# Performance work log

Hardware: AMD Instinct MI355X
Metric: run time of the kernel (lower is better)

## Reference

```python
import jax, jax.numpy as jnp
import numpy as np

N_NODES = 100000
N_EDGES = 1600000
D = 64
L = 3


def setup_inputs() -> dict:
    key = jax.random.key(0)
    ks = jax.random.split(key, 6)
    x = jax.random.normal(ks[0], (N_NODES, D), dtype=jnp.float32)
    edges = jax.random.randint(ks[1], (2, N_EDGES), 0, N_NODES, dtype=jnp.int64)
    scale = 1.0 / np.sqrt(D)
    W_phi = jax.random.normal(ks[2], (L, D, D), dtype=jnp.float32) * scale
    W_theta = jax.random.normal(ks[3], (L, D, D), dtype=jnp.float32) * scale
    W_out = jax.random.normal(ks[4], (1, D), dtype=jnp.float32) * scale
    b_out = jax.random.normal(ks[5], (1,), dtype=jnp.float32) * scale
    return {"x": x, "edges": edges, "W_phi": W_phi, "W_theta": W_theta,
            "W_out": W_out, "b_out": b_out}


def _devconv(x, Wp, Wt, src, dst):
    # DevConv: out_i = W_theta @ max_{j in N(i)} W_phi (x_j - x_i)
    diff = x[src] - x[dst]                 # [E, D] irregular gather
    msg = diff @ Wp.T                      # [E, D]
    agg = jax.ops.segment_max(msg, dst, num_segments=N_NODES)  # [N, D]
    agg = jnp.where(jnp.isneginf(agg), 0.0, agg)  # isolated nodes -> 0
    return agg @ Wt.T


def reference(x, edges, W_phi, W_theta, W_out, b_out):
    src, dst = edges[0], edges[1]
    for l in range(L):
        x = _devconv(x, W_phi[l], W_theta[l], src, dst)
    scores = (x @ W_out.T + b_out)[:, 0]   # Linear(D,1) then squeeze(-1)
    return jax.nn.sigmoid(scores)
```

## Files before the change

kernel.cpp:

```cpp
#include <hip/hip_runtime.h>
#include <math.h>


#define WBITS 9
#define WNODES 512
#define MAXNB 256
#define CHUNK 8192
#define STG_CAP 12288

#define PKNINF 0xFC00FC00u

typedef __fp16 h2v __attribute__((ext_vector_type(2)));
typedef _Float16 f16x8 __attribute__((ext_vector_type(8)));
typedef float f32x4 __attribute__((ext_vector_type(4)));

__device__ __forceinline__ unsigned pkmax(unsigned a, unsigned b) {
    unsigned r;
    asm("v_pk_max_f16 %0, %1, %2" : "=v"(r) : "v"(a), "v"(b));
    return r;
}
__device__ __forceinline__ unsigned pkrtz(float a, float b) {
    h2v r = __builtin_amdgcn_cvt_pkrtz(a, b);
    return *reinterpret_cast<unsigned*>(&r);
}
__device__ __forceinline__ float h2lo(unsigned u) {
    h2v h = *reinterpret_cast<h2v*>(&u);
    return (float)h.x;
}
__device__ __forceinline__ float h2hi(unsigned u) {
    h2v h = *reinterpret_cast<h2v*>(&u);
    return (float)h.y;
}

#define G8(K0) do { \
    int j0 = __builtin_amdgcn_ds_swizzle(myc, (((K0)+0)<<5)|0x10); \
    int j1 = __builtin_amdgcn_ds_swizzle(myc, (((K0)+1)<<5)|0x10); \
    int j2 = __builtin_amdgcn_ds_swizzle(myc, (((K0)+2)<<5)|0x10); \
    int j3 = __builtin_amdgcn_ds_swizzle(myc, (((K0)+3)<<5)|0x10); \
    int j4 = __builtin_amdgcn_ds_swizzle(myc, (((K0)+4)<<5)|0x10); \
    int j5 = __builtin_amdgcn_ds_swizzle(myc, (((K0)+5)<<5)|0x10); \
    int j6 = __builtin_amdgcn_ds_swizzle(myc, (((K0)+6)<<5)|0x10); \
    int j7 = __builtin_amdgcn_ds_swizzle(myc, (((K0)+7)<<5)|0x10); \
    uint2 w0 = y16[(size_t)j0 * 16 + t]; \
    uint2 w1 = y16[(size_t)j1 * 16 + t]; \
    uint2 w2 = y16[(size_t)j2 * 16 + t]; \
    uint2 w3 = y16[(size_t)j3 * 16 + t]; \
    uint2 w4 = y16[(size_t)j4 * 16 + t]; \
    uint2 w5 = y16[(size_t)j5 * 16 + t]; \
    uint2 w6 = y16[(size_t)j6 * 16 + t]; \
    uint2 w7 = y16[(size_t)j7 * 16 + t]; \
    c0 = pkmax(c0, pkmax(pkmax(pkmax(w0.x, w1.x), pkmax(w2.x, w3.x)), \
                         pkmax(pkmax(w4.x, w5.x), pkmax(w6.x, w7.x)))); \
    c1 = pkmax(c1, pkmax(pkmax(pkmax(w0.y, w1.y), pkmax(w2.y, w3.y)), \
                         pkmax(pkmax(w4.y, w5.y), pkmax(w6.y, w7.y)))); \
} while (0)

__global__ __launch_bounds__(256) void prep_k(
    const float* __restrict__ Wp, const float* __restrict__ Wt,
    const float* __restrict__ Wout,
    __fp16* __restrict__ Wh, float* __restrict__ vout)
{
    __shared__ float A[4096];
    __shared__ float B[4096];
    int tid = threadIdx.x;
    int b = blockIdx.x;
    if (b < 2) {
        const float* Ap = Wp + (size_t)(b + 1) * 4096;
        const float* Bp = Wt + (size_t)b * 4096;
        for (int i = tid; i < 4096; i += 256) { A[i] = Ap[i]; B[i] = Bp[i]; }
        __syncthreads();
        __fp16* C = Wh + (size_t)(b + 1) * 4096;
        for (int i = tid; i < 4096; i += 256) {
            int d = i >> 6, k = i & 63;
            float s = 0.f;
            #pragma unroll
            for (int m = 0; m < 64; ++m) s += A[d * 64 + m] * B[m * 64 + k];
            C[i] = (__fp16)s;
        }
    } else {
        for (int i = tid; i < 4096; i += 256) {
            A[i] = Wt[2 * 4096 + i];
            Wh[i] = (__fp16)Wp[i];
        }
        if (tid < 64) B[tid] = Wout[tid];
        __syncthreads();
        if (tid < 64) {
            float s = 0.f;
            #pragma unroll
            for (int m = 0; m < 64; ++m) s += B[m] * A[m * 64 + tid];
            vout[tid] = s;
        }
    }
}

__global__ __launch_bounds__(256) void clear_int_k(int* __restrict__ p, int n)
{
    int i = blockIdx.x * 256 + threadIdx.x;
    if (i < n) p[i] = 0;
}

__global__ __launch_bounds__(256) void bucket_hist_k(
    const int* __restrict__ eidx, int* __restrict__ bcnt, int E, int NB)
{
    __shared__ int h[MAXNB];
    int tid = threadIdx.x;
    for (int i = tid; i < NB; i += 256) h[i] = 0;
    __syncthreads();
    int start = blockIdx.x * CHUNK;
    int end = min(E, start + CHUNK);
    for (int e = start + tid; e < end; e += 256)
        atomicAdd(&h[eidx[E + e] >> WBITS], 1);
    __syncthreads();
    for (int i = tid; i < NB; i += 256)
        if (h[i]) atomicAdd(&bcnt[i], h[i]);
}

__global__ __launch_bounds__(256) void bucket_scan_k(
    const int* __restrict__ bcnt, int* __restrict__ bbase,
    int* __restrict__ gcur, int* __restrict__ row_ptr, int NB, int N, int E)
{
    __shared__ int sA[MAXNB], sB[MAXNB];
    int tid = threadIdx.x;
    int v0 = (tid < NB) ? bcnt[tid] : 0;
    sA[tid] = v0;
    __syncthreads();
    int* sp = sA; int* dp = sB;
    for (int off = 1; off < MAXNB; off <<= 1) {
        dp[tid] = sp[tid] + ((tid >= off) ? sp[tid - off] : 0);
        __syncthreads();
        int* t = sp; sp = dp; dp = t;
    }
    if (tid < NB) {
        int ex = sp[tid] - v0;
        bbase[tid] = ex;
        gcur[tid]  = ex;
    }
    if (tid == 0) {
        bbase[NB]  = E;
        row_ptr[N] = E;
    }
}

__global__ __launch_bounds__(256) void partA_k(
    const int* __restrict__ eidx, int* __restrict__ gcur,
    int* __restrict__ B1, int E, int NB)
{
    __shared__ int hist[MAXNB];
    __shared__ int lofs[MAXNB];
    __shared__ int lcur[MAXNB];
    __shared__ int gofs[MAXNB];
    __shared__ int sA[MAXNB], sB[MAXNB];
    __shared__ int stg_val[CHUNK];
    __shared__ int stg_pos[CHUNK];
    int tid = threadIdx.x;
    int start = blockIdx.x * CHUNK;
    int cnt = min(E - start, CHUNK);
    if (cnt <= 0) return;

    for (int i = tid; i < NB; i += 256) hist[i] = 0;
    __syncthreads();

    int es[CHUNK / 256], ed[CHUNK / 256];
    #pragma unroll
    for (int i = 0; i < CHUNK / 256; ++i) {
        int li = i * 256 + tid;
        if (li < cnt) {
            es[i] = eidx[start + li];
            ed[i] = eidx[E + start + li];
            atomicAdd(&hist[ed[i] >> WBITS], 1);
        }
    }
    __syncthreads();
    sA[tid] = (tid < NB) ? hist[tid] : 0;
    __syncthreads();
    int* sp = sA; int* dp = sB;
    for (int off = 1; off < MAXNB; off <<= 1) {
        dp[tid] = sp[tid] + ((tid >= off) ? sp[tid - off] : 0);
        __syncthreads();
        int* t = sp; sp = dp; dp = t;
    }
    if (tid < NB) {
        int c  = hist[tid];
        int ex = sp[tid] - c;
        lofs[tid] = ex;
        lcur[tid] = ex;
        gofs[tid] = c ? atomicAdd(&gcur[tid], c) : 0;
    }
    __syncthreads();
    #pragma unroll
    for (int i = 0; i < CHUNK / 256; ++i) {
        int li = i * 256 + tid;
        if (li < cnt) {
            int b = ed[i] >> WBITS;
            int p = atomicAdd(&lcur[b], 1);
            stg_val[p] = es[i] | ((ed[i] & (WNODES - 1)) << 17);
            stg_pos[p] = gofs[b] + (p - lofs[b]);
        }
    }
    __syncthreads();
    for (int i = tid; i < cnt; i += 256)
        B1[stg_pos[i]] = stg_val[i];
}

__global__ __launch_bounds__(256) void partB_k(
    const int* __restrict__ B1, const int* __restrict__ bbase,
    int* __restrict__ row_ptr, int* __restrict__ col, int N, int NB)
{
    __shared__ int cnt[WNODES];
    __shared__ int lcur[WNODES];
    __shared__ int sA[WNODES], sB[WNODES];
    __shared__ int stg[STG_CAP];
    int b   = blockIdx.x;
    int tid = threadIdx.x;
    int gb0 = bbase[b], gb1 = bbase[b + 1];
    int m   = gb1 - gb0;
    int nb0 = b << WBITS;

    for (int i = tid; i < WNODES; i += 256) cnt[i] = 0;
    __syncthreads();
    for (int i = tid; i < m; i += 256)
        atomicAdd(&cnt[B1[gb0 + i] >> 17], 1);
    __syncthreads();
    for (int i = tid; i < WNODES; i += 256) sA[i] = cnt[i];
    __syncthreads();
    int* sp = sA; int* dp = sB;
    for (int off = 1; off < WNODES; off <<= 1) {
        for (int i = tid; i < WNODES; i += 256)
            dp[i] = sp[i] + ((i >= off) ? sp[i - off] : 0);
        __syncthreads();
        int* t = sp; sp = dp; dp = t;
    }
    for (int i = tid; i < WNODES; i += 256) {
        int ex = sp[i] - cnt[i];
        lcur[i] = ex;
        int node = nb0 + i;
        if (node < N) row_ptr[node] = gb0 + ex;
    }
    __syncthreads();
    if (m <= STG_CAP) {
        for (int i = tid; i < m; i += 256) {
            int v = B1[gb0 + i];
            int p = atomicAdd(&lcur[v >> 17], 1);
            stg[p] = v & 0x1FFFF;
        }
        __syncthreads();
        for (int i = tid; i < m; i += 256)
            col[gb0 + i] = stg[i];
    } else {
        for (int i = tid; i < m; i += 256) {
            int v = B1[gb0 + i];
            int p = atomicAdd(&lcur[v >> 17], 1);
            col[gb0 + p] = v & 0x1FFFF;
        }
    }
}


__global__ __launch_bounds__(256) void gemm_mfma_k(
    const float* __restrict__ in, const __fp16* __restrict__ W,
    float* __restrict__ y32, unsigned short* __restrict__ y16, int n)
{
    int lane = threadIdx.x & 63;
    int wid  = threadIdx.x >> 6;
    int rt   = blockIdx.x * 4 + wid;
    int r0   = rt * 16;
    if (r0 >= n) return;

    int l15 = lane & 15;
    int ko  = (lane >> 4) * 8;

    f16x8 af[4][2];
    #pragma unroll
    for (int dt = 0; dt < 4; ++dt)
        #pragma unroll
        for (int kf = 0; kf < 2; ++kf)
            af[dt][kf] = *(const f16x8*)(W + (size_t)(dt * 16 + l15) * 64 + ko + kf * 32);

    f16x8 bf[2];
    #pragma unroll
    for (int kf = 0; kf < 2; ++kf) {
        const float4* p = (const float4*)(in + (size_t)(r0 + l15) * 64 + ko + kf * 32);
        float4 a = p[0], b = p[1];
        union { uint4 u; f16x8 h; } cv;
        cv.u.x = pkrtz(a.x, a.y); cv.u.y = pkrtz(a.z, a.w);
        cv.u.z = pkrtz(b.x, b.y); cv.u.w = pkrtz(b.z, b.w);
        bf[kf] = cv.h;
    }

    int r = r0 + l15;
    int d4 = (lane >> 4) * 4;
    #pragma unroll
    for (int dt = 0; dt < 4; ++dt) {
        f32x4 acc = {0.f, 0.f, 0.f, 0.f};
        acc = __builtin_amdgcn_mfma_f32_16x16x32_f16(af[dt][0], bf[0], acc, 0, 0, 0);
        acc = __builtin_amdgcn_mfma_f32_16x16x32_f16(af[dt][1], bf[1], acc, 0, 0, 0);
        int d = dt * 16 + d4;
        if (r < n) {
            float4 o; o.x = acc[0]; o.y = acc[1]; o.z = acc[2]; o.w = acc[3];
            *(float4*)(y32 + (size_t)r * 64 + d) = o;
            uint2 p; p.x = pkrtz(acc[0], acc[1]); p.y = pkrtz(acc[2], acc[3]);
            *(uint2*)(y16 + (size_t)r * 64 + d) = p;
        }
    }
}

template<bool HEAD>
__global__ __launch_bounds__(256) void gather_fused_k(
    const int* __restrict__ rp, const int* __restrict__ col,
    const uint2* __restrict__ y16, const float* y32,
    const __fp16* __restrict__ W,
    float* y32o, unsigned short* __restrict__ y16o,
    const float* __restrict__ vv, const float* __restrict__ bptr,
    float* __restrict__ out, int n)
{
    __shared__ __fp16 sAgg[4][16][80];
    int lane = threadIdx.x & 63;
    int wid  = threadIdx.x >> 6;
    int q = lane >> 4, t = lane & 15;
    int base = blockIdx.x * 64 + wid * 16;

    for (int p = 0; p < 4; ++p) {
        int node  = base + p * 4 + q;
        bool alive = node < n;
        int beg = 0, cnt = 0;
        if (alive) { beg = rp[node]; cnt = rp[node + 1] - beg; }
        unsigned c0 = PKNINF, c1 = PKNINF;
        if (cnt > 0) {
            int pcnt = (cnt + 7) & ~7;
            int e = 0;
            while (e < pcnt) {
                int myc = col[beg + min(e + t, cnt - 1)];
                G8(0);
                if (e + 8 < pcnt) { G8(8); }
                e += 16;
            }
        }
        if (alive) {
            bool has = cnt > 0;
            float4 yi = ((const float4*)y32)[(size_t)node * 16 + t];
            float g0 = has ? (h2lo(c0) - yi.x) : 0.f;
            float g1 = has ? (h2hi(c0) - yi.y) : 0.f;
            float g2 = has ? (h2lo(c1) - yi.z) : 0.f;
            float g3 = has ? (h2hi(c1) - yi.w) : 0.f;
            if (!HEAD) {
                uint2 pk; pk.x = pkrtz(g0, g1); pk.y = pkrtz(g2, g3);
                *(uint2*)&sAgg[wid][p * 4 + q][4 * t] = pk;
            } else {
                float4 vp = ((const float4*)vv)[t];
                float s = g0 * vp.x + g1 * vp.y + g2 * vp.z + g3 * vp.w;
                s += __shfl_xor(s, 8);
                s += __shfl_xor(s, 4);
                s += __shfl_xor(s, 2);
                s += __shfl_xor(s, 1);
                if (t == 0)
                    out[node] = 1.f / (1.f + __expf(-(s + bptr[0])));
            }
        } else if (!HEAD) {
            uint2 z; z.x = 0u; z.y = 0u;
            *(uint2*)&sAgg[wid][p * 4 + q][4 * t] = z;
        }
    }

    if (!HEAD) {
        __syncthreads();
        f16x8 af[4][2];
        #pragma unroll
        for (int dt = 0; dt < 4; ++dt)
            #pragma unroll
            for (int kf = 0; kf < 2; ++kf)
                af[dt][kf] = *(const f16x8*)(W + (size_t)(dt * 16 + t) * 64 + q * 8 + kf * 32);
        f16x8 bf[2];
        #pragma unroll
        for (int kf = 0; kf < 2; ++kf)
            bf[kf] = *(const f16x8*)&sAgg[wid][t][q * 8 + kf * 32];

        int r = base + t;
        int d4 = q * 4;
        #pragma unroll
        for (int dt = 0; dt < 4; ++dt) {
            f32x4 acc = {0.f, 0.f, 0.f, 0.f};
            acc = __builtin_amdgcn_mfma_f32_16x16x32_f16(af[dt][0], bf[0], acc, 0, 0, 0);
            acc = __builtin_amdgcn_mfma_f32_16x16x32_f16(af[dt][1], bf[1], acc, 0, 0, 0);
            if (r < n) {
                int d = dt * 16 + d4;
                float4 o; o.x = acc[0]; o.y = acc[1]; o.z = acc[2]; o.w = acc[3];
                *(float4*)(y32o + (size_t)r * 64 + d) = o;
                uint2 pk; pk.x = pkrtz(acc[0], acc[1]); pk.y = pkrtz(acc[2], acc[3]);
                *(uint2*)(y16o + (size_t)r * 64 + d) = pk;
            }
        }
    }
}

extern "C" void kernel_launch(void* const* d_in, const int* in_sizes, int n_in,
                              void* d_out, int out_size, void* d_ws, size_t ws_size,
                              hipStream_t stream)
{
    const float* x     = (const float*)d_in[0];
    const int*   edges = (const int*)d_in[1];
    const float* Wp    = (const float*)d_in[2];
    const float* Wt    = (const float*)d_in[3];
    const float* Wout  = (const float*)d_in[4];
    const float* bout  = (const float*)d_in[5];
    const int N = in_sizes[0] / 64;
    const int E = in_sizes[1] / 2;
    const int NB = (N + WNODES - 1) >> WBITS;
    float* out = (float*)d_out;

    char* ws = (char*)d_ws;
    float* y32 = (float*)ws; ws += (size_t)N * 64 * 4;
    int*   B1  = (int*)y32;
    unsigned short* y16A = (unsigned short*)ws; ws += (size_t)N * 64 * 2;
    unsigned short* y16B = (unsigned short*)ws; ws += (size_t)N * 64 * 2;
    int* col     = (int*)ws; ws += (size_t)(E + 8) * 4;
    int* row_ptr = (int*)ws; ws += (size_t)(N + 4) * 4;
    int* bcnt    = (int*)ws; ws += MAXNB * 4;
    int* bbase   = (int*)ws; ws += (MAXNB + 4) * 4;
    int* gcur    = (int*)ws; ws += MAXNB * 4;
    __fp16* Wh = (__fp16*)ws; ws += 3 * 4096 * 2;
    float*  vv = (float*)ws;  ws += 64 * 4;

    const int chunkBlocks = (E + CHUNK - 1) / CHUNK;
    const int gemmBlocks  = ((N + 15) / 16 + 3) / 4;
    const int fusedBlocks = (N + 63) / 64;

    prep_k<<<3, 256, 0, stream>>>(Wp, Wt, Wout, Wh, vv);

    clear_int_k<<<1, 256, 0, stream>>>(bcnt, NB);
    bucket_hist_k<<<chunkBlocks, 256, 0, stream>>>(edges, bcnt, E, NB);
    bucket_scan_k<<<1, 256, 0, stream>>>(bcnt, bbase, gcur, row_ptr, NB, N, E);
    partA_k<<<chunkBlocks, 256, 0, stream>>>(edges, gcur, B1, E, NB);
    partB_k<<<NB, 256, 0, stream>>>(B1, bbase, row_ptr, col, N, NB);

    gemm_mfma_k<<<gemmBlocks, 256, 0, stream>>>(x, Wh, y32, y16A, N);
    gather_fused_k<false><<<fusedBlocks, 256, 0, stream>>>(
        row_ptr, col, (const uint2*)y16A, y32, Wh + 4096, y32, y16B,
        nullptr, nullptr, nullptr, N);
    gather_fused_k<false><<<fusedBlocks, 256, 0, stream>>>(
        row_ptr, col, (const uint2*)y16B, y32, Wh + 8192, y32, y16A,
        nullptr, nullptr, nullptr, N);
    gather_fused_k<true><<<fusedBlocks, 256, 0, stream>>>(
        row_ptr, col, (const uint2*)y16A, y32, nullptr, nullptr, nullptr,
        vv, bout, out, N);
}
```

Baseline: 205.2 us.

## Drop fp32 activation buffer, fuse histogram with first GEMM, fold clear into prep

Removes the fp32 copy of each layer's transformed features. The self term x_i is now read from the fp16 buffer that is already written, which cuts a full-width write and read per layer. The edge-bucket histogram and the first-layer MFMA GEMM now run as one launch, split by block index, and clearing the bucket counts moves into the weight-prep kernel. Together these remove two launches, and the partition scratch B1 now aliases the second fp16 buffer. The trade-off is slightly lower precision in the x_i subtraction, since it now uses fp16 instead of fp32.

```diff
diff --git a/kernel.cpp b/kernel.cpp
--- a/kernel.cpp
+++ b/kernel.cpp
@@ -58,13 +58,15 @@
 __global__ __launch_bounds__(256) void prep_k(
     const float* __restrict__ Wp, const float* __restrict__ Wt,
     const float* __restrict__ Wout,
-    __fp16* __restrict__ Wh, float* __restrict__ vout)
+    __fp16* __restrict__ Wh, float* __restrict__ vout,
+    int* __restrict__ bcnt)
 {
     __shared__ float A[4096];
     __shared__ float B[4096];
     int tid = threadIdx.x;
     int b = blockIdx.x;
     if (b < 2) {
+        if (b == 0 && tid < MAXNB) bcnt[tid] = 0;
         const float* Ap = Wp + (size_t)(b + 1) * 4096;
         const float* Bp = Wt + (size_t)b * 4096;
         for (int i = tid; i < 4096; i += 256) { A[i] = Ap[i]; B[i] = Bp[i]; }
@@ -93,26 +95,64 @@
     }
 }
 
-__global__ __launch_bounds__(256) void clear_int_k(int* __restrict__ p, int n)
-{
-    int i = blockIdx.x * 256 + threadIdx.x;
-    if (i < n) p[i] = 0;
-}
-
-__global__ __launch_bounds__(256) void bucket_hist_k(
-    const int* __restrict__ eidx, int* __restrict__ bcnt, int E, int NB)
+__global__ __launch_bounds__(256) void hist_gemm_k(
+    const int* __restrict__ eidx, int* __restrict__ bcnt, int E, int NB,
+    int chunkBlocks,
+    const float* __restrict__ xin, const __fp16* __restrict__ W,
+    unsigned short* __restrict__ y16o, int n)
 {
     __shared__ int h[MAXNB];
     int tid = threadIdx.x;
-    for (int i = tid; i < NB; i += 256) h[i] = 0;
-    __syncthreads();
-    int start = blockIdx.x * CHUNK;
-    int end = min(E, start + CHUNK);
-    for (int e = start + tid; e < end; e += 256)
-        atomicAdd(&h[eidx[E + e] >> WBITS], 1);
-    __syncthreads();
-    for (int i = tid; i < NB; i += 256)
-        if (h[i]) atomicAdd(&bcnt[i], h[i]);
+    if (blockIdx.x < chunkBlocks) {
+        for (int i = tid; i < NB; i += 256) h[i] = 0;
+        __syncthreads();
+        int start = blockIdx.x * CHUNK;
+        int end = min(E, start + CHUNK);
+        for (int e = start + tid; e < end; e += 256)
+            atomicAdd(&h[eidx[E + e] >> WBITS], 1);
+        __syncthreads();
+        for (int i = tid; i < NB; i += 256)
+            if (h[i]) atomicAdd(&bcnt[i], h[i]);
+    } else {
+        int lane = tid & 63;
+        int wid  = tid >> 6;
+        int r0   = ((blockIdx.x - chunkBlocks) * 4 + wid) * 16;
+        if (r0 >= n) return;
+        int l15 = lane & 15;
+        int ko  = (lane >> 4) * 8;
+
+        f16x8 af[4][2];
+        #pragma unroll
+        for (int dt = 0; dt < 4; ++dt)
+            #pragma unroll
+            for (int kf = 0; kf < 2; ++kf)
+                af[dt][kf] = *(const f16x8*)(W + (size_t)(dt * 16 + l15) * 64 + ko + kf * 32);
+
+        f16x8 bf[2];
+        int rr = min(r0 + l15, n - 1);
+        #pragma unroll
+        for (int kf = 0; kf < 2; ++kf) {
+            const float4* p = (const float4*)(xin + (size_t)rr * 64 + ko + kf * 32);
+            float4 a = p[0], b = p[1];
+            union { uint4 u; f16x8 hh; } cv;
+            cv.u.x = pkrtz(a.x, a.y); cv.u.y = pkrtz(a.z, a.w);
+            cv.u.z = pkrtz(b.x, b.y); cv.u.w = pkrtz(b.z, b.w);
+            bf[kf] = cv.hh;
+        }
+
+        int r = r0 + l15;
+        int d4 = (lane >> 4) * 4;
+        #pragma unroll
+        for (int dt = 0; dt < 4; ++dt) {
+            f32x4 acc = {0.f, 0.f, 0.f, 0.f};
+            acc = __builtin_amdgcn_mfma_f32_16x16x32_f16(af[dt][0], bf[0], acc, 0, 0, 0);
+            acc = __builtin_amdgcn_mfma_f32_16x16x32_f16(af[dt][1], bf[1], acc, 0, 0, 0);
+            if (r < n) {
+                uint2 p; p.x = pkrtz(acc[0], acc[1]); p.y = pkrtz(acc[2], acc[3]);
+                *(uint2*)(y16o + (size_t)r * 64 + dt * 16 + d4) = p;
+            }
+        }
+    }
 }
 
 __global__ __launch_bounds__(256) void bucket_scan_k(
@@ -255,61 +295,12 @@
     }
 }
 
-
-__global__ __launch_bounds__(256) void gemm_mfma_k(
-    const float* __restrict__ in, const __fp16* __restrict__ W,
-    float* __restrict__ y32, unsigned short* __restrict__ y16, int n)
-{
-    int lane = threadIdx.x & 63;
-    int wid  = threadIdx.x >> 6;
-    int rt   = blockIdx.x * 4 + wid;
-    int r0   = rt * 16;
-    if (r0 >= n) return;
-
-    int l15 = lane & 15;
-    int ko  = (lane >> 4) * 8;
-
-    f16x8 af[4][2];
-    #pragma unroll
-    for (int dt = 0; dt < 4; ++dt)
-        #pragma unroll
-        for (int kf = 0; kf < 2; ++kf)
-            af[dt][kf] = *(const f16x8*)(W + (size_t)(dt * 16 + l15) * 64 + ko + kf * 32);
-
-    f16x8 bf[2];
-    #pragma unroll
-    for (int kf = 0; kf < 2; ++kf) {
-        const float4* p = (const float4*)(in + (size_t)(r0 + l15) * 64 + ko + kf * 32);
-        float4 a = p[0], b = p[1];
-        union { uint4 u; f16x8 h; } cv;
-        cv.u.x = pkrtz(a.x, a.y); cv.u.y = pkrtz(a.z, a.w);
-        cv.u.z = pkrtz(b.x, b.y); cv.u.w = pkrtz(b.z, b.w);
-        bf[kf] = cv.h;
-    }
-
-    int r = r0 + l15;
-    int d4 = (lane >> 4) * 4;
-    #pragma unroll
-    for (int dt = 0; dt < 4; ++dt) {
-        f32x4 acc = {0.f, 0.f, 0.f, 0.f};
-        acc = __builtin_amdgcn_mfma_f32_16x16x32_f16(af[dt][0], bf[0], acc, 0, 0, 0);
-        acc = __builtin_amdgcn_mfma_f32_16x16x32_f16(af[dt][1], bf[1], acc, 0, 0, 0);
-        int d = dt * 16 + d4;
-        if (r < n) {
-            float4 o; o.x = acc[0]; o.y = acc[1]; o.z = acc[2]; o.w = acc[3];
-            *(float4*)(y32 + (size_t)r * 64 + d) = o;
-            uint2 p; p.x = pkrtz(acc[0], acc[1]); p.y = pkrtz(acc[2], acc[3]);
-            *(uint2*)(y16 + (size_t)r * 64 + d) = p;
-        }
-    }
-}
-
 template<bool HEAD>
 __global__ __launch_bounds__(256) void gather_fused_k(
     const int* __restrict__ rp, const int* __restrict__ col,
-    const uint2* __restrict__ y16, const float* y32,
+    const uint2* __restrict__ y16,
     const __fp16* __restrict__ W,
-    float* y32o, unsigned short* __restrict__ y16o,
+    unsigned short* __restrict__ y16o,
     const float* __restrict__ vv, const float* __restrict__ bptr,
     float* __restrict__ out, int n)
 {
@@ -337,11 +328,11 @@
         }
         if (alive) {
             bool has = cnt > 0;
-            float4 yi = ((const float4*)y32)[(size_t)node * 16 + t];
-            float g0 = has ? (h2lo(c0) - yi.x) : 0.f;
-            float g1 = has ? (h2hi(c0) - yi.y) : 0.f;
-            float g2 = has ? (h2lo(c1) - yi.z) : 0.f;
-            float g3 = has ? (h2hi(c1) - yi.w) : 0.f;
+            uint2 yi2 = y16[(size_t)node * 16 + t];
+            float g0 = has ? (h2lo(c0) - h2lo(yi2.x)) : 0.f;
+            float g1 = has ? (h2hi(c0) - h2hi(yi2.x)) : 0.f;
+            float g2 = has ? (h2lo(c1) - h2lo(yi2.y)) : 0.f;
+            float g3 = has ? (h2hi(c1) - h2hi(yi2.y)) : 0.f;
             if (!HEAD) {
                 uint2 pk; pk.x = pkrtz(g0, g1); pk.y = pkrtz(g2, g3);
                 *(uint2*)&sAgg[wid][p * 4 + q][4 * t] = pk;
@@ -382,11 +373,8 @@
             acc = __builtin_amdgcn_mfma_f32_16x16x32_f16(af[dt][0], bf[0], acc, 0, 0, 0);
             acc = __builtin_amdgcn_mfma_f32_16x16x32_f16(af[dt][1], bf[1], acc, 0, 0, 0);
             if (r < n) {
-                int d = dt * 16 + d4;
-                float4 o; o.x = acc[0]; o.y = acc[1]; o.z = acc[2]; o.w = acc[3];
-                *(float4*)(y32o + (size_t)r * 64 + d) = o;
                 uint2 pk; pk.x = pkrtz(acc[0], acc[1]); pk.y = pkrtz(acc[2], acc[3]);
-                *(uint2*)(y16o + (size_t)r * 64 + d) = pk;
+                *(uint2*)(y16o + (size_t)r * 64 + dt * 16 + d4) = pk;
             }
         }
     }
@@ -408,10 +396,9 @@
     float* out = (float*)d_out;
 
     char* ws = (char*)d_ws;
-    float* y32 = (float*)ws; ws += (size_t)N * 64 * 4;
-    int*   B1  = (int*)y32;
     unsigned short* y16A = (unsigned short*)ws; ws += (size_t)N * 64 * 2;
     unsigned short* y16B = (unsigned short*)ws; ws += (size_t)N * 64 * 2;
+    int*   B1  = (int*)y16B;
     int* col     = (int*)ws; ws += (size_t)(E + 8) * 4;
     int* row_ptr = (int*)ws; ws += (size_t)(N + 4) * 4;
     int* bcnt    = (int*)ws; ws += MAXNB * 4;
@@ -424,22 +411,21 @@
     const int gemmBlocks  = ((N + 15) / 16 + 3) / 4;
     const int fusedBlocks = (N + 63) / 64;
 
-    prep_k<<<3, 256, 0, stream>>>(Wp, Wt, Wout, Wh, vv);
-
-    clear_int_k<<<1, 256, 0, stream>>>(bcnt, NB);
-    bucket_hist_k<<<chunkBlocks, 256, 0, stream>>>(edges, bcnt, E, NB);
+    prep_k<<<3, 256, 0, stream>>>(Wp, Wt, Wout, Wh, vv, bcnt);
+
+    hist_gemm_k<<<chunkBlocks + gemmBlocks, 256, 0, stream>>>(
+        edges, bcnt, E, NB, chunkBlocks, x, Wh, y16A, N);
     bucket_scan_k<<<1, 256, 0, stream>>>(bcnt, bbase, gcur, row_ptr, NB, N, E);
     partA_k<<<chunkBlocks, 256, 0, stream>>>(edges, gcur, B1, E, NB);
     partB_k<<<NB, 256, 0, stream>>>(B1, bbase, row_ptr, col, N, NB);
 
-    gemm_mfma_k<<<gemmBlocks, 256, 0, stream>>>(x, Wh, y32, y16A, N);
     gather_fused_k<false><<<fusedBlocks, 256, 0, stream>>>(
-        row_ptr, col, (const uint2*)y16A, y32, Wh + 4096, y32, y16B,
+        row_ptr, col, (const uint2*)y16A, Wh + 4096, y16B,
         nullptr, nullptr, nullptr, N);
     gather_fused_k<false><<<fusedBlocks, 256, 0, stream>>>(
-        row_ptr, col, (const uint2*)y16B, y32, Wh + 8192, y32, y16A,
+        row_ptr, col, (const uint2*)y16B, Wh + 8192, y16A,
         nullptr, nullptr, nullptr, N);
     gather_fused_k<true><<<fusedBlocks, 256, 0, stream>>>(
-        row_ptr, col, (const uint2*)y16A, y32, nullptr, nullptr, nullptr,
+        row_ptr, col, (const uint2*)y16A, nullptr, nullptr,
         vv, bout, out, N);
 }
```

New measurement: 181.2 us. 1.13x faster.
